# Performance work log

Measured on AMD Instinct MI355X. Metric: run time of the kernel, lower is better.

Reference implementation:

```python
import jax, jax.numpy as jnp
import numpy as np

C = 8           # feat_channel
B, N = 8, 64    # batch, max objects
H, W = 128, 128
D = (C + 2) * C + C + C * C + C + C + 1  # 169


def setup_inputs() -> dict:
    key = jax.random.key(0)
    k1, k2, k3, k4 = jax.random.split(key, 4)
    seg_feat = jax.random.normal(k1, (B, C, H, W), dtype=jnp.float32)
    conv_weight = jax.random.normal(k2, (B, D, H, W), dtype=jnp.float32)
    mask = jnp.ones((B, N), dtype=jnp.float32)
    ind = jax.random.randint(k3, (B, N), 0, H * W, dtype=jnp.int64)
    target = jax.random.uniform(k4, (B, N, H, W), dtype=jnp.float32)
    return {"seg_feat": seg_feat, "conv_weight": conv_weight, "mask": mask,
            "ind": ind, "target": target}


def reference(seg_feat, conv_weight, mask, ind, target):
    b, c, h, w = seg_feat.shape
    n = ind.shape[1]
    # _tranpose_and_gather_feat: [B,D,H,W] -> [B,HW,D] -> gather at ind -> [B,N,D]
    wflat = conv_weight.reshape(b, -1, h * w).transpose(0, 2, 1)
    weight = jnp.take_along_axis(wflat, ind[:, :, None], axis=1)  # [B,N,D]
    splits = np.cumsum([(c + 2) * c, c, c * c, c, c])
    w1, b1, w2, b2, w3, b3 = jnp.split(weight, splits, axis=-1)
    w1 = w1.reshape(b, n, c, c + 2)   # per-object conv1 1x1 weights
    w2 = w2.reshape(b, n, c, c)
    w3 = w3.reshape(b, n, 1, c)
    # object centers and relative coordinate maps
    x0 = (ind % w).astype(jnp.float32)
    y0 = (ind // w).astype(jnp.float32)
    xg = jnp.arange(w, dtype=jnp.float32)
    yg = jnp.arange(h, dtype=jnp.float32)
    y_grid, x_grid = jnp.meshgrid(yg, xg, indexing="ij")  # [H,W]
    x_rel = (x_grid[None, None] - x0[:, :, None, None]) / 128.0  # [B,N,H,W]
    y_rel = (y_grid[None, None] - y0[:, :, None, None]) / 128.0
    feat = jnp.concatenate(
        [jnp.broadcast_to(seg_feat[:, None], (b, n, c, h, w)),
         x_rel[:, :, None], y_rel[:, :, None]], axis=2)  # [B,N,C+2,H,W]
    # three grouped 1x1 convs == per-object channel contractions
    h1 = jax.nn.relu(jnp.einsum("bnoc,bnchw->bnohw", w1, feat) + b1[..., None, None])
    h2 = jax.nn.relu(jnp.einsum("bnoc,bnchw->bnohw", w2, h1) + b2[..., None, None])
    out = jax.nn.sigmoid(jnp.einsum("bnoc,bnchw->bnohw", w3, h2) + b3[..., None, None])[:, :, 0]  # [B,N,H,W]
    m = mask[:, :, None, None]
    pred = out * m
    tgt = target * m
    smooth = 1.0
    inter = jnp.sum(pred * tgt, axis=(1, 2, 3))
    denom = jnp.sum(pred * pred, axis=(1, 2, 3)) + jnp.sum(tgt * tgt, axis=(1, 2, 3))
    loss = 1.0 - (2.0 * inter + smooth) / (denom + smooth)  # per-image dice
    return jnp.mean(loss)  # sum over batch / batch_size
```

## Files before the change

kernel.cpp:

```cpp
#include <hip/hip_runtime.h>

#define Cc 8
#define Hh 128
#define Ww 128
#define Nn 64
#define Bb 8
#define Dd 169
#define HW (Hh * Ww)
#define CHUNKS 4
#define NBLK (Bb * Nn * CHUNKS)
#define PXB (HW / CHUNKS)
#define GROUPS 4

#define INV128 (1.0f / 128.0f)

typedef __fp16 f16x2 __attribute__((ext_vector_type(2)));

static __device__ __forceinline__ f16x2 pk(float a, float b) {
    return __builtin_amdgcn_cvt_pkrtz(a, b);
}
static __device__ __forceinline__ uint32_t pku(float a, float b) {
    f16x2 t = pk(a, b); uint32_t u; __builtin_memcpy(&u, &t, 4); return u;
}
static __device__ __forceinline__ f16x2 u2h(uint32_t u) {
    f16x2 r; __builtin_memcpy(&r, &u, 4); return r;
}
static __device__ __forceinline__ uint32_t rfl(uint32_t x) {
    return __builtin_amdgcn_readfirstlane(x);
}

#if __has_builtin(__builtin_amdgcn_fdot2)
static __device__ __forceinline__ float dot2(uint32_t w, f16x2 f, float acc) {
    return __builtin_amdgcn_fdot2(u2h(w), f, acc, false);
}
#else
static __device__ __forceinline__ float dot2(uint32_t w, f16x2 f, float acc) {
    f16x2 wv = u2h(w);
    return acc + (float)wv.x * (float)f.x + (float)wv.y * (float)f.y;
}
#endif

static __device__ __forceinline__ float pick(float4 v, int j) {
    return j == 0 ? v.x : j == 1 ? v.y : j == 2 ? v.z : v.w;
}

__global__ __launch_bounds__(256)
void seg_dice_main(const float* __restrict__ seg_feat,
                   const float* __restrict__ conv_weight,
                   const float* __restrict__ mask,
                   const int*   __restrict__ ind,
                   const float* __restrict__ target,
                   float* __restrict__ ws) {
    const int g     = (blockIdx.x & 7) * (NBLK / 8) + (blockIdx.x >> 3);
    const int bn    = g >> 2;
    const int chunk = g & (CHUNKS - 1);
    const int b     = bn >> 6;
    const int tid   = threadIdx.x;

    __shared__ float w_s[Dd];
    const int ind_bn = ind[bn];

    for (int i = tid; i < Dd; i += 256)
        w_s[i] = conv_weight[(size_t)b * Dd * HW + (size_t)i * HW + ind_bn];
    __syncthreads();

    uint32_t pw1[40];
    #pragma unroll
    for (int j = 0; j < 40; ++j) pw1[j] = rfl(pku(w_s[2 * j], w_s[2 * j + 1]));
    uint32_t pw2[32];
    #pragma unroll
    for (int j = 0; j < 32; ++j) pw2[j] = rfl(pku(w_s[88 + 2 * j], w_s[89 + 2 * j]));
    uint32_t pw3[4];
    #pragma unroll
    for (int j = 0; j < 4; ++j)  pw3[j] = rfl(pku(w_s[160 + 2 * j], w_s[161 + 2 * j]));
    float b1f[8], b2f[8];
    #pragma unroll
    for (int o = 0; o < 8; ++o) { b1f[o] = w_s[80 + o]; b2f[o] = w_s[152 + o]; }
    const float b3f = w_s[168];

    const float m  = mask[bn];
    const float x0 = (float)(ind_bn & (Ww - 1));
    const float y0 = (float)(ind_bn >> 7);

    const float* seg_b  = seg_feat + (size_t)b * Cc * HW;
    const float* tgt_bn = target   + (size_t)bn * HW;

    float inter = 0.f, ps = 0.f, ts = 0.f;
    const int pbase = chunk * PXB + (tid << 2);

    #pragma unroll 1
    for (int it = 0; it < GROUPS; ++it) {
        const int p = pbase + (it << 10);

        const float4 t4 = *(const float4*)(tgt_bn + p);
        float4 f4[8];
        #pragma unroll
        for (int c = 0; c < 8; ++c) f4[c] = *(const float4*)(seg_b + c * HW + p);

        const float yrf = ((float)(p >> 7)        - y0) * INV128;
        const float xbf = ((float)(p & (Ww - 1)) - x0) * INV128;

        #pragma unroll
        for (int j = 0; j < 4; ++j) {
            const f16x2 fp0 = pk(pick(f4[0], j), pick(f4[1], j));
            const f16x2 fp1 = pk(pick(f4[2], j), pick(f4[3], j));
            const f16x2 fp2 = pk(pick(f4[4], j), pick(f4[5], j));
            const f16x2 fp3 = pk(pick(f4[6], j), pick(f4[7], j));
            const f16x2 fpx = pk(xbf + (float)j * INV128, yrf);

            float h1[8];
            #pragma unroll
            for (int o = 0; o < 8; ++o) {
                float a = b1f[o];
                a = dot2(pw1[5 * o + 0], fp0, a);
                a = dot2(pw1[5 * o + 1], fp1, a);
                a = dot2(pw1[5 * o + 2], fp2, a);
                a = dot2(pw1[5 * o + 3], fp3, a);
                a = dot2(pw1[5 * o + 4], fpx, a);
                h1[o] = fmaxf(a, 0.f);
            }
            const f16x2 hp0 = pk(h1[0], h1[1]);
            const f16x2 hp1 = pk(h1[2], h1[3]);
            const f16x2 hp2 = pk(h1[4], h1[5]);
            const f16x2 hp3 = pk(h1[6], h1[7]);

            float h2[8];
            #pragma unroll
            for (int o = 0; o < 8; ++o) {
                float a = b2f[o];
                a = dot2(pw2[4 * o + 0], hp0, a);
                a = dot2(pw2[4 * o + 1], hp1, a);
                a = dot2(pw2[4 * o + 2], hp2, a);
                a = dot2(pw2[4 * o + 3], hp3, a);
                h2[o] = fmaxf(a, 0.f);
            }
            const f16x2 gp0 = pk(h2[0], h2[1]);
            const f16x2 gp1 = pk(h2[2], h2[3]);
            const f16x2 gp2 = pk(h2[4], h2[5]);
            const f16x2 gp3 = pk(h2[6], h2[7]);

            float z = b3f;
            z = dot2(pw3[0], gp0, z);
            z = dot2(pw3[1], gp1, z);
            z = dot2(pw3[2], gp2, z);
            z = dot2(pw3[3], gp3, z);

            const float o_ = __builtin_amdgcn_rcpf(1.f + __expf(-z));
            const float tv = pick(t4, j);
            inter = fmaf(o_, tv, inter);
            ps    = fmaf(o_, o_, ps);
            ts    = fmaf(tv, tv, ts);
        }
    }

    const float m2 = m * m;
    inter *= m2; ps *= m2; ts *= m2;

    #pragma unroll
    for (int off = 32; off > 0; off >>= 1) {
        inter += __shfl_down(inter, off);
        ps    += __shfl_down(ps,    off);
        ts    += __shfl_down(ts,    off);
    }
    __shared__ float red[3][4];
    const int wave = tid >> 6;
    if ((tid & 63) == 0) { red[0][wave] = inter; red[1][wave] = ps; red[2][wave] = ts; }
    __syncthreads();
    if (tid == 0) {
        const int local = (bn & 63) * CHUNKS + chunk;
        ws[(b * 3 + 0) * 256 + local] = red[0][0] + red[0][1] + red[0][2] + red[0][3];
        ws[(b * 3 + 1) * 256 + local] = red[1][0] + red[1][1] + red[1][2] + red[1][3];
        ws[(b * 3 + 2) * 256 + local] = red[2][0] + red[2][1] + red[2][2] + red[2][3];
    }
}

__global__ void seg_dice_final(const float* __restrict__ ws, float* __restrict__ out) {
    __shared__ float red[24][4];
    const int tid = threadIdx.x;
    if (tid < 96) {
        const int series = tid >> 2;
        const int part   = tid & 3;
        const float4* p = (const float4*)(ws + series * 256 + part * 64);
        float s = 0.f;
        #pragma unroll
        for (int i = 0; i < 16; ++i) { const float4 v = p[i]; s += (v.x + v.y) + (v.z + v.w); }
        red[series][part] = s;
    }
    __syncthreads();
    if (tid == 0) {
        float acc = 0.f;
        #pragma unroll
        for (int b = 0; b < Bb; ++b) {
            const float inter = red[b*3+0][0] + red[b*3+0][1] + red[b*3+0][2] + red[b*3+0][3];
            const float p2    = red[b*3+1][0] + red[b*3+1][1] + red[b*3+1][2] + red[b*3+1][3];
            const float t2    = red[b*3+2][0] + red[b*3+2][1] + red[b*3+2][2] + red[b*3+2][3];
            acc += 1.0f - (2.0f * inter + 1.0f) / (p2 + t2 + 1.0f);
        }
        out[0] = acc * (1.0f / (float)Bb);
    }
}

extern "C" void kernel_launch(void* const* d_in, const int* in_sizes, int n_in,
                              void* d_out, int out_size, void* d_ws, size_t ws_size,
                              hipStream_t stream) {
    const float* seg_feat    = (const float*)d_in[0];
    const float* conv_weight = (const float*)d_in[1];
    const float* mask        = (const float*)d_in[2];
    const int*   ind         = (const int*)d_in[3];
    const float* target      = (const float*)d_in[4];
    float* out = (float*)d_out;
    float* ws  = (float*)d_ws;

    seg_dice_main<<<NBLK, 256, 0, stream>>>(seg_feat, conv_weight, mask, ind, target, ws);
    seg_dice_final<<<1, 128, 0, stream>>>(ws, out);
}
```

Before: 43.66 us.

## Pre-pack per-object fp16 weights in a separate kernel before main pass

Adds a pack_weights kernel that gathers each object's 169 weights from conv_weight once and stores them as packed fp16 pairs in a compact per-object table. The main kernel then loads this table with vectorized uint4 loads instead of doing a strided scattered gather, a shared-memory barrier and fp16 conversion in each of the 4 chunk blocks. This removes redundant gathers (4x per object) and the sync, at the cost of an extra kernel launch. Biases are now also rounded to fp16, and dropping readfirstlane may leave the weights in vector registers instead of scalar ones, raising register pressure.

New measurement: 45.36 us. +3.9%, slower.

```diff
diff --git a/kernel.cpp b/kernel.cpp
--- a/kernel.cpp
+++ b/kernel.cpp
@@ -11,6 +11,8 @@
 #define NBLK (Bb * Nn * CHUNKS)
 #define PXB (HW / CHUNKS)
 #define GROUPS 4
+#define WSTRIDE 88
+#define RED_OFF (Bb * Nn * WSTRIDE)
 
 #define INV128 (1.0f / 128.0f)
 
@@ -24,9 +26,6 @@
 }
 static __device__ __forceinline__ f16x2 u2h(uint32_t u) {
     f16x2 r; __builtin_memcpy(&r, &u, 4); return r;
-}
-static __device__ __forceinline__ uint32_t rfl(uint32_t x) {
-    return __builtin_amdgcn_readfirstlane(x);
 }
 
 #if __has_builtin(__builtin_amdgcn_fdot2)
@@ -44,40 +43,60 @@
     return j == 0 ? v.x : j == 1 ? v.y : j == 2 ? v.z : v.w;
 }
 
+__global__ void pack_weights(const float* __restrict__ conv_weight,
+                             const int*   __restrict__ ind,
+                             uint32_t*    __restrict__ wt) {
+    const int bn = blockIdx.x;
+    const int j  = threadIdx.x;
+    const int b  = bn >> 6;
+    const int ind_bn = ind[bn];
+    const float* src = conv_weight + (size_t)b * Dd * HW + ind_bn;
+    if (j < 85) {
+        int d0, d1;
+        if (j < 40)      { d0 = (j / 5) * 10 + (j % 5) * 2; d1 = d0 + 1; }
+        else if (j < 72) { d0 = 88  + 2 * (j - 40); d1 = d0 + 1; }
+        else if (j < 76) { d0 = 160 + 2 * (j - 72); d1 = d0 + 1; }
+        else if (j < 80) { d0 = 80  + 2 * (j - 76); d1 = d0 + 1; }
+        else if (j < 84) { d0 = 152 + 2 * (j - 80); d1 = d0 + 1; }
+        else             { d0 = 168; d1 = -1; }
+        const float a = src[(size_t)d0 * HW];
+        const float c = (d1 >= 0) ? src[(size_t)d1 * HW] : 0.f;
+        wt[bn * WSTRIDE + j] = pku(a, c);
+    }
+}
+
 __global__ __launch_bounds__(256)
 void seg_dice_main(const float* __restrict__ seg_feat,
-                   const float* __restrict__ conv_weight,
                    const float* __restrict__ mask,
                    const int*   __restrict__ ind,
                    const float* __restrict__ target,
-                   float* __restrict__ ws) {
+                   const uint32_t* __restrict__ wtab,
+                   float* __restrict__ red_base) {
     const int g     = (blockIdx.x & 7) * (NBLK / 8) + (blockIdx.x >> 3);
     const int bn    = g >> 2;
     const int chunk = g & (CHUNKS - 1);
     const int b     = bn >> 6;
     const int tid   = threadIdx.x;
 
-    __shared__ float w_s[Dd];
-    const int ind_bn = ind[bn];
-
-    for (int i = tid; i < Dd; i += 256)
-        w_s[i] = conv_weight[(size_t)b * Dd * HW + (size_t)i * HW + ind_bn];
-    __syncthreads();
-
-    uint32_t pw1[40];
-    #pragma unroll
-    for (int j = 0; j < 40; ++j) pw1[j] = rfl(pku(w_s[2 * j], w_s[2 * j + 1]));
-    uint32_t pw2[32];
-    #pragma unroll
-    for (int j = 0; j < 32; ++j) pw2[j] = rfl(pku(w_s[88 + 2 * j], w_s[89 + 2 * j]));
-    uint32_t pw3[4];
-    #pragma unroll
-    for (int j = 0; j < 4; ++j)  pw3[j] = rfl(pku(w_s[160 + 2 * j], w_s[161 + 2 * j]));
+    uint32_t wq[88];
+    {
+        const uint4* wt4 = (const uint4*)(wtab + bn * WSTRIDE);
+        #pragma unroll
+        for (int k = 0; k < 22; ++k) {
+            const uint4 q = wt4[k];
+            wq[4 * k + 0] = q.x; wq[4 * k + 1] = q.y;
+            wq[4 * k + 2] = q.z; wq[4 * k + 3] = q.w;
+        }
+    }
     float b1f[8], b2f[8];
     #pragma unroll
-    for (int o = 0; o < 8; ++o) { b1f[o] = w_s[80 + o]; b2f[o] = w_s[152 + o]; }
-    const float b3f = w_s[168];
-
+    for (int k = 0; k < 4; ++k) {
+        const f16x2 v1 = u2h(wq[76 + k]); b1f[2 * k] = (float)v1.x; b1f[2 * k + 1] = (float)v1.y;
+        const f16x2 v2 = u2h(wq[80 + k]); b2f[2 * k] = (float)v2.x; b2f[2 * k + 1] = (float)v2.y;
+    }
+    const float b3f = (float)u2h(wq[84]).x;
+
+    const int   ind_bn = ind[bn];
     const float m  = mask[bn];
     const float x0 = (float)(ind_bn & (Ww - 1));
     const float y0 = (float)(ind_bn >> 7);
@@ -112,11 +131,11 @@
             #pragma unroll
             for (int o = 0; o < 8; ++o) {
                 float a = b1f[o];
-                a = dot2(pw1[5 * o + 0], fp0, a);
-                a = dot2(pw1[5 * o + 1], fp1, a);
-                a = dot2(pw1[5 * o + 2], fp2, a);
-                a = dot2(pw1[5 * o + 3], fp3, a);
-                a = dot2(pw1[5 * o + 4], fpx, a);
+                a = dot2(wq[5 * o + 0], fp0, a);
+                a = dot2(wq[5 * o + 1], fp1, a);
+                a = dot2(wq[5 * o + 2], fp2, a);
+                a = dot2(wq[5 * o + 3], fp3, a);
+                a = dot2(wq[5 * o + 4], fpx, a);
                 h1[o] = fmaxf(a, 0.f);
             }
             const f16x2 hp0 = pk(h1[0], h1[1]);
@@ -128,10 +147,10 @@
             #pragma unroll
             for (int o = 0; o < 8; ++o) {
                 float a = b2f[o];
-                a = dot2(pw2[4 * o + 0], hp0, a);
-                a = dot2(pw2[4 * o + 1], hp1, a);
-                a = dot2(pw2[4 * o + 2], hp2, a);
-                a = dot2(pw2[4 * o + 3], hp3, a);
+                a = dot2(wq[40 + 4 * o + 0], hp0, a);
+                a = dot2(wq[40 + 4 * o + 1], hp1, a);
+                a = dot2(wq[40 + 4 * o + 2], hp2, a);
+                a = dot2(wq[40 + 4 * o + 3], hp3, a);
                 h2[o] = fmaxf(a, 0.f);
             }
             const f16x2 gp0 = pk(h2[0], h2[1]);
@@ -140,10 +159,10 @@
             const f16x2 gp3 = pk(h2[6], h2[7]);
 
             float z = b3f;
-            z = dot2(pw3[0], gp0, z);
-            z = dot2(pw3[1], gp1, z);
-            z = dot2(pw3[2], gp2, z);
-            z = dot2(pw3[3], gp3, z);
+            z = dot2(wq[72], gp0, z);
+            z = dot2(wq[73], gp1, z);
+            z = dot2(wq[74], gp2, z);
+            z = dot2(wq[75], gp3, z);
 
             const float o_ = __builtin_amdgcn_rcpf(1.f + __expf(-z));
             const float tv = pick(t4, j);
@@ -168,19 +187,19 @@
     __syncthreads();
     if (tid == 0) {
         const int local = (bn & 63) * CHUNKS + chunk;
-        ws[(b * 3 + 0) * 256 + local] = red[0][0] + red[0][1] + red[0][2] + red[0][3];
-        ws[(b * 3 + 1) * 256 + local] = red[1][0] + red[1][1] + red[1][2] + red[1][3];
-        ws[(b * 3 + 2) * 256 + local] = red[2][0] + red[2][1] + red[2][2] + red[2][3];
-    }
-}
-
-__global__ void seg_dice_final(const float* __restrict__ ws, float* __restrict__ out) {
+        red_base[(b * 3 + 0) * 256 + local] = red[0][0] + red[0][1] + red[0][2] + red[0][3];
+        red_base[(b * 3 + 1) * 256 + local] = red[1][0] + red[1][1] + red[1][2] + red[1][3];
+        red_base[(b * 3 + 2) * 256 + local] = red[2][0] + red[2][1] + red[2][2] + red[2][3];
+    }
+}
+
+__global__ void seg_dice_final(const float* __restrict__ red_base, float* __restrict__ out) {
     __shared__ float red[24][4];
     const int tid = threadIdx.x;
     if (tid < 96) {
         const int series = tid >> 2;
         const int part   = tid & 3;
-        const float4* p = (const float4*)(ws + series * 256 + part * 64);
+        const float4* p = (const float4*)(red_base + series * 256 + part * 64);
         float s = 0.f;
         #pragma unroll
         for (int i = 0; i < 16; ++i) { const float4 v = p[i]; s += (v.x + v.y) + (v.z + v.w); }
@@ -211,6 +230,10 @@
     float* out = (float*)d_out;
     float* ws  = (float*)d_ws;
 
-    seg_dice_main<<<NBLK, 256, 0, stream>>>(seg_feat, conv_weight, mask, ind, target, ws);
-    seg_dice_final<<<1, 128, 0, stream>>>(ws, out);
-}
+    uint32_t* wtab     = (uint32_t*)ws;
+    float*    red_base = ws + RED_OFF;
+
+    pack_weights<<<Bb * Nn, 96, 0, stream>>>(conv_weight, ind, wtab);
+    seg_dice_main<<<NBLK, 256, 0, stream>>>(seg_feat, mask, ind, target, wtab, red_base);
+    seg_dice_final<<<1, 128, 0, stream>>>(red_base, out);
+}
```
